# Performance work log

Hardware: AMD Instinct MI355X
Metric: run time of the kernel (lower is better)

## Reference

```python
import jax, jax.numpy as jnp
import numpy as np

N = 100000      # nodes
E_RAND = 1500000
IN_DIM = 128
OUT_DIM = 128
H = 8
D = OUT_DIM // H  # 16 per-head dim
EPS = 1e-5


def _bn(x, gamma, beta):
    # BatchNorm1d, training mode: biased batch statistics over the node dim
    mu = jnp.mean(x, axis=0)
    var = jnp.mean((x - mu) ** 2, axis=0)
    return (x - mu) * jax.lax.rsqrt(var + EPS) * gamma + beta


def setup_inputs() -> dict:
    key = jax.random.key(0)
    ks = jax.random.split(key, 12)
    h = jax.random.normal(ks[0], (N, IN_DIM), dtype=jnp.float32)
    # edge list: random edges + self-loops so every dst has in-degree >= 1
    src_r = jax.random.randint(ks[1], (E_RAND,), 0, N, dtype=jnp.int32)
    dst_r = jax.random.randint(ks[2], (E_RAND,), 0, N, dtype=jnp.int32)
    loops = jnp.arange(N, dtype=jnp.int32)
    src = jnp.concatenate([loops, src_r])
    dst = jnp.concatenate([loops, dst_r])
    s = 1.0 / np.sqrt(IN_DIM)
    Wq = jax.random.normal(ks[3], (IN_DIM, OUT_DIM), dtype=jnp.float32) * s
    Wk = jax.random.normal(ks[4], (IN_DIM, OUT_DIM), dtype=jnp.float32) * s
    Wv = jax.random.normal(ks[5], (IN_DIM, OUT_DIM), dtype=jnp.float32) * s
    Wo = jax.random.normal(ks[6], (OUT_DIM, OUT_DIM), dtype=jnp.float32) * s
    bo = jnp.zeros((OUT_DIM,), dtype=jnp.float32)
    gamma1 = jnp.ones((OUT_DIM,), dtype=jnp.float32)
    beta1 = jnp.zeros((OUT_DIM,), dtype=jnp.float32)
    Wf1 = jax.random.normal(ks[7], (OUT_DIM, 2 * OUT_DIM), dtype=jnp.float32) * s
    bf1 = jnp.zeros((2 * OUT_DIM,), dtype=jnp.float32)
    Wf2 = jax.random.normal(ks[8], (2 * OUT_DIM, OUT_DIM), dtype=jnp.float32) * (1.0 / np.sqrt(2 * OUT_DIM))
    bf2 = jnp.zeros((OUT_DIM,), dtype=jnp.float32)
    gamma2 = jnp.ones((OUT_DIM,), dtype=jnp.float32)
    beta2 = jnp.zeros((OUT_DIM,), dtype=jnp.float32)
    return {"h": h, "Wq": Wq, "Wk": Wk, "Wv": Wv, "Wo": Wo, "bo": bo,
            "gamma1": gamma1, "beta1": beta1, "Wf1": Wf1, "bf1": bf1,
            "Wf2": Wf2, "bf2": bf2, "gamma2": gamma2, "beta2": beta2,
            "src": src, "dst": dst}


def reference(h, Wq, Wk, Wv, Wo, bo, gamma1, beta1, Wf1, bf1, Wf2, bf2,
              gamma2, beta2, src, dst):
    n = h.shape[0]
    Q = (h @ Wq).reshape(n, H, D)
    K = (h @ Wk).reshape(n, H, D)
    V = (h @ Wv).reshape(n, H, D)
    # per-edge score: (K[src] * Q[dst]).sum(-1), scaled exp with clamp
    score = jnp.sum(K[src] * Q[dst], axis=-1) / np.sqrt(D)   # [E, H]
    score = jnp.exp(jnp.clip(score, -5.0, 5.0))
    # weighted aggregation to dst nodes
    wV = jax.ops.segment_sum(V[src] * score[:, :, None], dst, num_segments=n)  # [N,H,D]
    z = jax.ops.segment_sum(score, dst, num_segments=n)                         # [N,H]
    attn = (wV / z[:, :, None]).reshape(n, OUT_DIM)
    # output projection + residual + batchnorm
    x = h + (attn @ Wo + bo)
    x = _bn(x, gamma1, beta1)
    # FFN + residual + batchnorm
    y = jax.nn.relu(x @ Wf1 + bf1) @ Wf2 + bf2
    x = _bn(x + y, gamma2, beta2)
    return x
```

## Files before the change

### kernel.cpp

```cpp
#include <hip/hip_runtime.h>

#define EPS 1e-5f
#define VSCALE 20.0f

typedef __attribute__((ext_vector_type(8))) short sh8;
typedef __attribute__((ext_vector_type(4))) float f4;
typedef __attribute__((ext_vector_type(2))) _Float16 h2f;

static __device__ __forceinline__ unsigned short f2b(float f) {
    union { float f; unsigned u; } v; v.f = f;
    unsigned r = v.u + 0x7FFF + ((v.u >> 16) & 1);
    return (unsigned short)(r >> 16);
}
static __device__ __forceinline__ float b2f(unsigned short b) {
    union { unsigned u; float f; } v; v.u = ((unsigned)b) << 16; return v.f;
}
static __device__ __forceinline__ unsigned pk2(float a, float b) {
    return (unsigned)f2b(a) | ((unsigned)f2b(b) << 16);
}
static __device__ __forceinline__ h2f u2h(unsigned u) {
    union { unsigned u; h2f h; } c; c.u = u; return c.h;
}
static __device__ __forceinline__ float dot2h(h2f a, h2f b, float c) {
#if __has_builtin(__builtin_amdgcn_fdot2)
    return __builtin_amdgcn_fdot2(a, b, c, false);
#else
    return (float)a.x * (float)b.x + (float)a.y * (float)b.y + c;
#endif
}
#if __has_builtin(__builtin_amdgcn_cvt_f32_ubyte0)
#define UB0(x) __builtin_amdgcn_cvt_f32_ubyte0(x)
#define UB1(x) __builtin_amdgcn_cvt_f32_ubyte1(x)
#define UB2(x) __builtin_amdgcn_cvt_f32_ubyte2(x)
#define UB3(x) __builtin_amdgcn_cvt_f32_ubyte3(x)
#else
#define UB0(x) ((float)((x) & 0xffu))
#define UB1(x) ((float)(((x) >> 8) & 0xffu))
#define UB2(x) ((float)(((x) >> 16) & 0xffu))
#define UB3(x) ((float)((x) >> 24))
#endif

static __device__ __forceinline__ void barrier_raw() {
    __builtin_amdgcn_sched_barrier(0);
    asm volatile("s_waitcnt lgkmcnt(0)" ::: "memory");
    __builtin_amdgcn_s_barrier();
    __builtin_amdgcn_sched_barrier(0);
}

__global__ __launch_bounds__(256) void prep_all_k(
    const float* __restrict__ Wq, const float* __restrict__ Wk,
    const float* __restrict__ Wv, const float* __restrict__ Wo,
    const float* __restrict__ Wf1, const float* __restrict__ Wf2,
    unsigned short* __restrict__ Wt)
{
    int i = blockIdx.x * 256 + threadIdx.x;
    if (i < 65536) {
        int s = i >> 14;
        const float* W = (s == 0) ? Wq : (s == 1) ? Wk : (s == 2) ? Wv : Wo;
        int l = i & 16383, k = l >> 7, n = l & 127;
        Wt[(i & ~16383) + n * 128 + k] = f2b(W[l]);
    } else if (i < 98304) {
        int l = i - 65536, k = l >> 8, n = l & 255;
        Wt[65536 + n * 128 + k] = f2b(Wf1[l]);
    } else {
        int l = i - 98304, k = l >> 7, n = l & 127;
        Wt[98304 + n * 256 + k] = f2b(Wf2[l]);
    }
}

__global__ __launch_bounds__(256) void qkv_k(
    const float* __restrict__ h, const unsigned short* __restrict__ Wt,
    _Float16* __restrict__ Qh, unsigned char* __restrict__ KV, int M)
{
    __shared__ __align__(16) unsigned short As[128 * 136];
    __shared__ __align__(16) unsigned short Ws[128 * 72];
    const int tid = threadIdx.x;
    const int wave = tid >> 6, lane = tid & 63;
    const int q = lane >> 4, lm = lane & 15;
    const int rowBase = blockIdx.x * 128;
    const int r0 = (wave & 1) * 64, c0 = (wave >> 1) * 64;

#pragma unroll
    for (int j = 0; j < 16; ++j) {
        int idx = tid + j * 256;
        int row = idx >> 5, kk = (idx & 31) * 4;
        int grow = rowBase + row;
        float4 v = make_float4(0.f, 0.f, 0.f, 0.f);
        if (grow < M) v = *(const float4*)&h[(size_t)grow * 128 + kk];
        ushort4 b;
        b.x = f2b(v.x); b.y = f2b(v.y); b.z = f2b(v.z); b.w = f2b(v.w);
        *(ushort4*)&As[row * 136 + kk] = b;
    }

    for (int w = 0; w < 3; ++w) {
        f4 acc[4][4];
#pragma unroll
        for (int mi = 0; mi < 4; ++mi)
#pragma unroll
            for (int ni = 0; ni < 4; ++ni) {
                f4 z = {0.f, 0.f, 0.f, 0.f};
                acc[mi][ni] = z;
            }
        for (int kc = 0; kc < 2; ++kc) {
#pragma unroll
            for (int j = 0; j < 4; ++j) {
                int idx = tid + j * 256;
                int n = idx >> 3, kk = (idx & 7) * 8;
                uint4 v = *(const uint4*)&Wt[(size_t)w * 16384 + (size_t)n * 128 + kc * 64 + kk];
                *(uint4*)&Ws[n * 72 + kk] = v;
            }
            __syncthreads();
#pragma unroll
            for (int k2 = 0; k2 < 2; ++k2) {
                sh8 af[4], bfr[4];
#pragma unroll
                for (int t = 0; t < 4; ++t) {
                    af[t]  = *(const sh8*)&As[(r0 + t * 16 + lm) * 136 + kc * 64 + k2 * 32 + q * 8];
                    bfr[t] = *(const sh8*)&Ws[(c0 + t * 16 + lm) * 72 + k2 * 32 + q * 8];
                }
#pragma unroll
                for (int mi = 0; mi < 4; ++mi)
#pragma unroll
                    for (int ni = 0; ni < 4; ++ni)
                        acc[mi][ni] = __builtin_amdgcn_mfma_f32_16x16x32_bf16(
                            af[mi], bfr[ni], acc[mi][ni], 0, 0, 0);
            }
            __syncthreads();
        }
#pragma unroll
        for (int mi = 0; mi < 4; ++mi)
#pragma unroll
            for (int ni = 0; ni < 4; ++ni) {
                const int col = c0 + ni * 16 + lm;
#pragma unroll
                for (int r = 0; r < 4; ++r) {
                    int grow = rowBase + r0 + mi * 16 + q * 4 + r;
                    if (grow >= M) continue;
                    const float v = acc[mi][ni][r];
                    if (w == 0) Qh[(size_t)grow * 128 + col] = (_Float16)v;
                    else if (w == 1)
                        *(_Float16*)(KV + (size_t)grow * 384 + col * 2) = (_Float16)v;
                    else {
                        float t = rintf(v * VSCALE);
                        t = fminf(fmaxf(t, -127.f), 127.f);
                        KV[(size_t)grow * 384 + 256 + col] = (unsigned char)(int)(t + 128.f);
                    }
                }
            }
    }
}

template<int KD, int RES, int STATS, int RELU>
__global__ __launch_bounds__(512) void gemm2_k(
    const unsigned short* __restrict__ A, const unsigned short* __restrict__ Wt,
    const float* __restrict__ bias, const void* __restrict__ resid,
    unsigned short* __restrict__ C, int M, int ldc, int tiles,
    const float* __restrict__ aff1, float* __restrict__ ostats)
{
    constexpr int CPR = KD / 8;
    constexpr int PER = 64 * CPR / 512;
    __shared__ __align__(16) unsigned short Ws[128 * KD];
    __shared__ __align__(16) unsigned short As[2][64 * KD];
    __shared__ float sacc[256];
    const int tid = threadIdx.x;
    const int wave = tid >> 6, lane = tid & 63;
    const int q = lane >> 4, lm = lane & 15;
    const int wr = wave >> 2, wc = wave & 3;
    const int colBase = blockIdx.y * 128;
    const unsigned short* Wblk = Wt + (size_t)colBase * KD;

    uint4 rA[PER];
    {
        const int rowT = blockIdx.x * 64;
#pragma unroll
        for (int i = 0; i < PER; ++i) {
            int g = tid + i * 512;
            int row = g / CPR, ch = g % CPR;
            int grow = rowT + row; if (grow >= M) grow = M - 1;
            rA[i] = *(const uint4*)&A[(size_t)grow * KD + ch * 8];
        }
    }

#pragma unroll
    for (int i = 0; i < 128 * CPR / 512; ++i) {
        int g = tid + i * 512;
        int col = g / CPR, ch = g % CPR;
        uint4 v = *(const uint4*)&Wblk[(size_t)col * KD + ch * 8];
        *(uint4*)&Ws[col * KD + ((ch ^ (col & 7)) * 8)] = v;
    }
    if (STATS && tid < 256) sacc[tid] = 0.f;

    float bv[2], rsc[2], rsh[2];
#pragma unroll
    for (int ni = 0; ni < 2; ++ni) {
        const int col = colBase + wc * 32 + ni * 16 + lm;
        bv[ni] = bias[col];
        if (RES == 3) { rsc[ni] = aff1[col]; rsh[ni] = aff1[128 + col]; }
        else { rsc[ni] = 0.f; rsh[ni] = 0.f; }
    }
    float st_s[2] = {0.f, 0.f}, st_ss[2] = {0.f, 0.f};

    int cur = 0;
    for (int t = blockIdx.x; t < tiles; t += gridDim.x) {
        const int rowT = t * 64;
        barrier_raw();
        unsigned short* Asc = As[cur];
#pragma unroll
        for (int i = 0; i < PER; ++i) {
            int g = tid + i * 512;
            int row = g / CPR, ch = g % CPR;
            *(uint4*)&Asc[row * KD + ((ch ^ (row & 7)) * 8)] = rA[i];
        }
        const int tn = t + (int)gridDim.x;
        if (tn < tiles) {
            const int rowTn = tn * 64;
#pragma unroll
            for (int i = 0; i < PER; ++i) {
                int g = tid + i * 512;
                int row = g / CPR, ch = g % CPR;
                int grow = rowTn + row; if (grow >= M) grow = M - 1;
                rA[i] = *(const uint4*)&A[(size_t)grow * KD + ch * 8];
            }
        }
        barrier_raw();

        f4 acc[2][2];
#pragma unroll
        for (int mi = 0; mi < 2; ++mi)
#pragma unroll
            for (int ni = 0; ni < 2; ++ni) {
                f4 z = {0.f, 0.f, 0.f, 0.f};
                acc[mi][ni] = z;
            }
#pragma unroll
        for (int kc = 0; kc < KD / 32; ++kc) {
            sh8 af[2], bfr[2];
#pragma unroll
            for (int mi = 0; mi < 2; ++mi) {
                const int row = wr * 32 + mi * 16 + lm;
                af[mi] = *(const sh8*)&Asc[row * KD + (((kc * 4 + q) ^ (row & 7)) * 8)];
            }
#pragma unroll
            for (int ni = 0; ni < 2; ++ni) {
                const int col = wc * 32 + ni * 16 + lm;
                bfr[ni] = *(const sh8*)&Ws[col * KD + (((kc * 4 + q) ^ (col & 7)) * 8)];
            }
#pragma unroll
            for (int mi = 0; mi < 2; ++mi)
#pragma unroll
                for (int ni = 0; ni < 2; ++ni)
                    acc[mi][ni] = __builtin_amdgcn_mfma_f32_16x16x32_bf16(
                        af[mi], bfr[ni], acc[mi][ni], 0, 0, 0);
        }

#pragma unroll
        for (int ni = 0; ni < 2; ++ni) {
            const int col = colBase + wc * 32 + ni * 16 + lm;
#pragma unroll
            for (int mi = 0; mi < 2; ++mi) {
#pragma unroll
                for (int r = 0; r < 4; ++r) {
                    const int row = rowT + wr * 32 + mi * 16 + q * 4 + r;
                    if (row >= M) continue;
                    float val = acc[mi][ni][r] + bv[ni];
                    if (RES == 1)
                        val += ((const float*)resid)[(size_t)row * ldc + col];
                    if (RES == 3)
                        val += b2f(((const unsigned short*)resid)[(size_t)row * ldc + col])
                               * rsc[ni] + rsh[ni];
                    if (RELU) val = fmaxf(val, 0.f);
                    if (STATS) { st_s[ni] += val; st_ss[ni] += val * val; }
                    C[(size_t)row * ldc + col] = f2b(val);
                }
            }
        }
        cur ^= 1;
    }

    if (STATS) {
        barrier_raw();
#pragma unroll
        for (int ni = 0; ni < 2; ++ni) {
            st_s[ni]  += __shfl_xor(st_s[ni], 16);  st_s[ni]  += __shfl_xor(st_s[ni], 32);
            st_ss[ni] += __shfl_xor(st_ss[ni], 16); st_ss[ni] += __shfl_xor(st_ss[ni], 32);
            if (q == 0) {
                const int c = wc * 32 + ni * 16 + lm;
                atomicAdd(&sacc[c], st_s[ni]);
                atomicAdd(&sacc[128 + c], st_ss[ni]);
            }
        }
        barrier_raw();
        if (tid < 128) {
            atomicAdd(&ostats[tid], sacc[tid]);
            atomicAdd(&ostats[128 + tid], sacc[128 + tid]);
        }
    }
}

__global__ __launch_bounds__(256) void fold_bn1_k(
    const unsigned short* __restrict__ W1t, const float* __restrict__ rstats,
    const float* __restrict__ g1, const float* __restrict__ b1,
    const float* __restrict__ bf1, float invN,
    unsigned short* __restrict__ W1f, float* __restrict__ b1f,
    float* __restrict__ aff1)
{
    __shared__ float sc[128], sh[128];
    const int t = threadIdx.x;
    if (t < 128) {
        const float mu = rstats[t] * invN;
        const float var = rstats[128 + t] * invN - mu * mu;
        const float isg = rsqrtf(var + EPS) * g1[t];
        const float shf = b1[t] - mu * isg;
        sc[t] = isg; sh[t] = shf;
        aff1[t] = isg; aff1[128 + t] = shf;
    }
    __syncthreads();
    float acc = bf1[t];
#pragma unroll
    for (int c = 0; c < 128; c += 8) {
        const uint4 v = *(const uint4*)&W1t[t * 128 + c];
        const float w0 = b2f((unsigned short)(v.x & 0xffff));
        const float w1 = b2f((unsigned short)(v.x >> 16));
        const float w2 = b2f((unsigned short)(v.y & 0xffff));
        const float w3 = b2f((unsigned short)(v.y >> 16));
        const float w4 = b2f((unsigned short)(v.z & 0xffff));
        const float w5 = b2f((unsigned short)(v.z >> 16));
        const float w6 = b2f((unsigned short)(v.w & 0xffff));
        const float w7 = b2f((unsigned short)(v.w >> 16));
        acc += sh[c] * w0 + sh[c + 1] * w1 + sh[c + 2] * w2 + sh[c + 3] * w3
             + sh[c + 4] * w4 + sh[c + 5] * w5 + sh[c + 6] * w6 + sh[c + 7] * w7;
        uint4 o;
        o.x = pk2(w0 * sc[c],     w1 * sc[c + 1]);
        o.y = pk2(w2 * sc[c + 2], w3 * sc[c + 3]);
        o.z = pk2(w4 * sc[c + 4], w5 * sc[c + 5]);
        o.w = pk2(w6 * sc[c + 6], w7 * sc[c + 7]);
        *(uint4*)&W1f[t * 128 + c] = o;
    }
    b1f[t] = acc;
}

__global__ __launch_bounds__(256) void bucket_cnt_k(const int* __restrict__ dst,
                                                    int E, int* __restrict__ bCnt)
{
    __shared__ int c[512];
    const int t = threadIdx.x;
    c[t] = 0; c[t + 256] = 0;
    __syncthreads();
    for (int i = blockIdx.x * 256 + t; i < E; i += gridDim.x * 256)
        atomicAdd(&c[dst[i] >> 8], 1);
    __syncthreads();
    if (c[t]) atomicAdd(&bCnt[t], c[t]);
    if (c[t + 256]) atomicAdd(&bCnt[t + 256], c[t + 256]);
}

__global__ __launch_bounds__(512) void bucket_scan_k(const int* __restrict__ bCnt,
                                                     int B, int* __restrict__ bOff,
                                                     int* __restrict__ bCur)
{
    __shared__ int ts[512];
    const int t = threadIdx.x;
    const int v = (t < B) ? bCnt[t] : 0;
    ts[t] = v;
    __syncthreads();
    for (int o = 1; o < 512; o <<= 1) {
        int u = (t >= o) ? ts[t - o] : 0;
        __syncthreads();
        ts[t] += u;
        __syncthreads();
    }
    const int ex = ts[t] - v;
    if (t < B) { bOff[t] = ex; bCur[t] = ex; }
    if (t == B - 1) bOff[B] = ex + v;
}

#define CCH 8192
__global__ __launch_bounds__(512) void coarse_k(const int* __restrict__ src,
                                                const int* __restrict__ dst, int E,
                                                int* __restrict__ bCur,
                                                unsigned* __restrict__ coarse)
{
    __shared__ int cnt[512], off[512], gbase[512], rc[512];
    __shared__ unsigned pk[CCH];
    __shared__ int ga[CCH];
    const int t = threadIdx.x;
    const int e0 = blockIdx.x * CCH;
    const int n = min(CCH, E - e0);
    cnt[t] = 0;
    __syncthreads();
    for (int i = t; i < n; i += 512) atomicAdd(&cnt[dst[e0 + i] >> 8], 1);
    __syncthreads();
    const int v = cnt[t];
    off[t] = v;
    __syncthreads();
    for (int o = 1; o < 512; o <<= 1) {
        int u = (t >= o) ? off[t - o] : 0;
        __syncthreads();
        off[t] += u;
        __syncthreads();
    }
    const int ex = off[t] - v;
    off[t] = ex;
    if (v > 0) gbase[t] = atomicAdd(&bCur[t], v);
    rc[t] = 0;
    __syncthreads();
    for (int i = t; i < n; i += 512) {
        const int d = dst[e0 + i], s = src[e0 + i];
        const int b = d >> 8;
        const int j = atomicAdd(&rc[b], 1);
        const int slot = off[b] + j;
        pk[slot] = ((unsigned)(d & 255) << 17) | (unsigned)s;
        ga[slot] = gbase[b] + j;
    }
    __syncthreads();
    for (int i = t; i < n; i += 512) coarse[ga[i]] = pk[i];
}

__global__ __launch_bounds__(256) void fine_k(const unsigned* __restrict__ coarse,
                                              const int* __restrict__ bOff, int B,
                                              int Nn, int* __restrict__ row_ptr,
                                              int* __restrict__ esrc)
{
    __shared__ int cnt[256], off[256], rc[256];
    const int t = threadIdx.x;
    const int b = blockIdx.x;
    const int base = b << 8;
    const int e0 = bOff[b], e1 = bOff[b + 1];
    cnt[t] = 0;
    __syncthreads();
    for (int i = e0 + t; i < e1; i += 256)
        atomicAdd(&cnt[(coarse[i] >> 17) & 255], 1);
    __syncthreads();
    const int v = cnt[t];
    off[t] = v;
    __syncthreads();
    for (int o = 1; o < 256; o <<= 1) {
        int u = (t >= o) ? off[t - o] : 0;
        __syncthreads();
        off[t] += u;
        __syncthreads();
    }
    const int ex = off[t] - v;
    off[t] = ex;
    rc[t] = 0;
    if (base + t < Nn) row_ptr[base + t] = e0 + ex;
    if (b == B - 1 && t == 0) row_ptr[Nn] = e1;
    __syncthreads();
    for (int i = e0 + t; i < e1; i += 256) {
        const unsigned p = coarse[i];
        const int l = (p >> 17) & 255;
        const int j = atomicAdd(&rc[l], 1);
        esrc[e0 + off[l] + j] = (int)(p & 0x1FFFFu);
    }
}

#define EA_ACC(kc, vc, EI) do {                                              \
    float sp = dot2h(u2h((kc).w), q3, dot2h(u2h((kc).z), q2,                 \
               dot2h(u2h((kc).y), q1, dot2h(u2h((kc).x), q0, 0.f))));        \
    sp += __shfl_xor(sp, 1);                                                 \
    float sc = __expf(fminf(fmaxf(sp * 0.25f, -5.f), 5.f));                  \
    sc = ((EI) < nb) ? sc : 0.f;                                             \
    a0 += sc * UB0((vc).x);                                                  \
    a1 += sc * UB1((vc).x);                                                  \
    a2 += sc * UB2((vc).x);                                                  \
    a3 += sc * UB3((vc).x);                                                  \
    a4 += sc * UB0((vc).y);                                                  \
    a5 += sc * UB1((vc).y);                                                  \
    a6 += sc * UB2((vc).y);                                                  \
    a7 += sc * UB3((vc).y);                                                  \
    z += sc;                                                                 \
} while (0)

__global__ __launch_bounds__(256) void edge_attn_k(
    const _Float16* __restrict__ Qh, const unsigned char* __restrict__ KV,
    const int* __restrict__ row_ptr, const int* __restrict__ esrc,
    unsigned short* __restrict__ attnb, int Nn)
{
    const int wave = threadIdx.x >> 6, lane = threadIdx.x & 63;
    const int node = blockIdx.x * 4 + wave;
    if (node >= Nn) return;
    const int g = lane & 15, p = lane >> 4;
    const uint4 qv = *(const uint4*)&Qh[(size_t)node * 128 + g * 8];
    const h2f q0 = u2h(qv.x), q1 = u2h(qv.y), q2 = u2h(qv.z), q3 = u2h(qv.w);
    const int e0 = row_ptr[node], e1 = row_ptr[node + 1];
    const int cnt = e1 - e0;
    const int e1m1 = e1 - 1;
    float a0 = 0.f, a1 = 0.f, a2 = 0.f, a3 = 0.f;
    float a4 = 0.f, a5 = 0.f, a6 = 0.f, a7 = 0.f, z = 0.f;
    for (int base = 0; base < cnt; base += 64) {
        const int nb = min(cnt - base, 64);
        const int eb = e0 + base + p;
        {
            const int s0 = esrc[min(eb, e1m1)];
            const unsigned char* r = KV + (size_t)((unsigned)s0 * 384u);
            const int s1 = esrc[min(eb + 4, e1m1)];
            const unsigned char* rB = KV + (size_t)((unsigned)s1 * 384u);
            uint4 kvA = *(const uint4*)(r + g * 16);
            uint2 vvA = *(const uint2*)(r + 256 + g * 8);
            uint4 kvB = *(const uint4*)(rB + g * 16);
            uint2 vvB = *(const uint2*)(rB + 256 + g * 8);
            for (int j = 0; j < nb; j += 8) {
                {
                    const uint4 kc = kvA; const uint2 vc = vvA;
                    if (j + 8 < nb) {
                        const int sn = esrc[min(eb + j + 8, e1m1)];
                        const unsigned char* rn = KV + (size_t)((unsigned)sn * 384u);
                        kvA = *(const uint4*)(rn + g * 16);
                        vvA = *(const uint2*)(rn + 256 + g * 8);
                    }
                    EA_ACC(kc, vc, j + p);
                }
                {
                    const uint4 kc = kvB; const uint2 vc = vvB;
                    if (j + 12 < nb) {
                        const int sn = esrc[min(eb + j + 12, e1m1)];
                        const unsigned char* rn = KV + (size_t)((unsigned)sn * 384u);
                        kvB = *(const uint4*)(rn + g * 16);
                        vvB = *(const uint2*)(rn + 256 + g * 8);
                    }
                    EA_ACC(kc, vc, j + 4 + p);
                }
            }
        }
    }
    a0 += __shfl_xor(a0, 16); a0 += __shfl_xor(a0, 32);
    a1 += __shfl_xor(a1, 16); a1 += __shfl_xor(a1, 32);
    a2 += __shfl_xor(a2, 16); a2 += __shfl_xor(a2, 32);
    a3 += __shfl_xor(a3, 16); a3 += __shfl_xor(a3, 32);
    a4 += __shfl_xor(a4, 16); a4 += __shfl_xor(a4, 32);
    a5 += __shfl_xor(a5, 16); a5 += __shfl_xor(a5, 32);
    a6 += __shfl_xor(a6, 16); a6 += __shfl_xor(a6, 32);
    a7 += __shfl_xor(a7, 16); a7 += __shfl_xor(a7, 32);
    z  += __shfl_xor(z, 16);  z  += __shfl_xor(z, 32);
    const float inv = 1.f / (z * VSCALE);
    const float c = 128.f * z;
    if (p == 0) {
        uint4 o;
        o.x = pk2((a0 - c) * inv, (a1 - c) * inv);
        o.y = pk2((a2 - c) * inv, (a3 - c) * inv);
        o.z = pk2((a4 - c) * inv, (a5 - c) * inv);
        o.w = pk2((a6 - c) * inv, (a7 - c) * inv);
        *(uint4*)&attnb[(size_t)node * 128 + g * 8] = o;
    }
}

__global__ __launch_bounds__(256) void bn_apply_b_k(const unsigned short* __restrict__ X,
                                                    const float* __restrict__ rstats,
                                                    const float* __restrict__ gma,
                                                    const float* __restrict__ bta,
                                                    float invN, int total8,
                                                    float* __restrict__ out)
{
    __shared__ float aff[256];
    if (threadIdx.x < 128) {
        const int c = threadIdx.x;
        const float mu = rstats[c] * invN;
        const float var = rstats[128 + c] * invN - mu * mu;
        const float isg = rsqrtf(var + EPS) * gma[c];
        aff[c] = isg;
        aff[128 + c] = bta[c] - mu * isg;
    }
    __syncthreads();
    for (int i = blockIdx.x * blockDim.x + threadIdx.x; i < total8;
         i += gridDim.x * blockDim.x) {
        const int c8 = (i & 15) * 8;
        const float4 sc0 = *(const float4*)&aff[c8];
        const float4 sc1 = *(const float4*)&aff[c8 + 4];
        const float4 sh0 = *(const float4*)&aff[128 + c8];
        const float4 sh1 = *(const float4*)&aff[128 + c8 + 4];
        const uint4 v = ((const uint4*)X)[i];
        float4 o0, o1;
        o0.x = b2f((unsigned short)(v.x & 0xffff)) * sc0.x + sh0.x;
        o0.y = b2f((unsigned short)(v.x >> 16))    * sc0.y + sh0.y;
        o0.z = b2f((unsigned short)(v.y & 0xffff)) * sc0.z + sh0.z;
        o0.w = b2f((unsigned short)(v.y >> 16))    * sc0.w + sh0.w;
        o1.x = b2f((unsigned short)(v.z & 0xffff)) * sc1.x + sh1.x;
        o1.y = b2f((unsigned short)(v.z >> 16))    * sc1.y + sh1.y;
        o1.z = b2f((unsigned short)(v.w & 0xffff)) * sc1.z + sh1.z;
        o1.w = b2f((unsigned short)(v.w >> 16))    * sc1.w + sh1.w;
        ((float4*)out)[i * 2]     = o0;
        ((float4*)out)[i * 2 + 1] = o1;
    }
}

extern "C" void kernel_launch(void* const* d_in, const int* in_sizes, int n_in,
                              void* d_out, int out_size, void* d_ws, size_t ws_size,
                              hipStream_t stream)
{
    const float* h   = (const float*)d_in[0];
    const float* Wq  = (const float*)d_in[1];
    const float* Wk  = (const float*)d_in[2];
    const float* Wv  = (const float*)d_in[3];
    const float* Wo  = (const float*)d_in[4];
    const float* bo  = (const float*)d_in[5];
    const float* g1  = (const float*)d_in[6];
    const float* b1  = (const float*)d_in[7];
    const float* Wf1 = (const float*)d_in[8];
    const float* bf1 = (const float*)d_in[9];
    const float* Wf2 = (const float*)d_in[10];
    const float* bf2 = (const float*)d_in[11];
    const float* g2  = (const float*)d_in[12];
    const float* b2  = (const float*)d_in[13];
    const int*   src = (const int*)d_in[14];
    const int*   dstv= (const int*)d_in[15];
    const int N = in_sizes[0] / 128;
    const int E = in_sizes[14];
    const int B = (N + 255) >> 8;
    const float invN = 1.f / (float)N;

    unsigned short* Wt = (unsigned short*)d_ws;
    float* stats1 = (float*)((char*)d_ws + 262144);
    float* stats2 = stats1 + 256;
    int* bCnt = (int*)(stats2 + 256);
    int* bOff = bCnt + 512;
    int* bCur = bOff + 513;
    uintptr_t big = ((uintptr_t)(bCur + 512) + 255) & ~(uintptr_t)255;
    _Float16* Qh = (_Float16*)big;
    unsigned char* KV = (unsigned char*)(Qh + (size_t)N * 128);
    uintptr_t a2 = ((uintptr_t)(KV + (size_t)N * 384) + 255) & ~(uintptr_t)255;
    unsigned short* attnb = (unsigned short*)a2;
    unsigned short* xb = attnb + (size_t)N * 128;
    int* row_ptr = (int*)(xb + (size_t)N * 128);
    unsigned* coarse = (unsigned*)attnb;
    int* esrc = (int*)xb;
    unsigned short* hidden = (unsigned short*)Qh;
    unsigned short* yb = attnb;
    uintptr_t fb = (big + (size_t)N * 512 + 255) & ~(uintptr_t)255;
    float* aff1 = (float*)fb;
    float* b1f  = aff1 + 256;
    unsigned short* W1f = (unsigned short*)(b1f + 256);

    unsigned short* Wf1T = Wt + 65536;
    unsigned short* Wf2T = Wt + 98304;

    float* out = (float*)d_out;
    const dim3 b256(256);
    const dim3 b512(512);
    const int tiles128 = (N + 127) / 128;
    const int tiles64 = (N + 63) / 64;

    hipMemsetAsync(stats1, 0, 4096, stream);

    prep_all_k<<<dim3(512), b256, 0, stream>>>(Wq, Wk, Wv, Wo, Wf1, Wf2, Wt);

    bucket_cnt_k<<<dim3(256), b256, 0, stream>>>(dstv, E, bCnt);
    bucket_scan_k<<<dim3(1), dim3(512), 0, stream>>>(bCnt, B, bOff, bCur);
    coarse_k<<<dim3((E + CCH - 1) / CCH), dim3(512), 0, stream>>>(src, dstv, E, bCur, coarse);
    fine_k<<<dim3(B), b256, 0, stream>>>(coarse, bOff, B, N, row_ptr, esrc);

    qkv_k<<<dim3(tiles128), b256, 0, stream>>>(h, Wt, Qh, KV, N);

    edge_attn_k<<<dim3((N + 3) / 4), b256, 0, stream>>>(Qh, KV, row_ptr, esrc, attnb, N);

    gemm2_k<128, 1, 1, 0><<<dim3(512, 1), b512, 0, stream>>>(
        attnb, Wt + 49152, bo, h, xb, N, 128, tiles64, nullptr, stats1);

    fold_bn1_k<<<dim3(1), b256, 0, stream>>>(Wf1T, stats1, g1, b1, bf1, invN,
                                             W1f, b1f, aff1);

    gemm2_k<128, 0, 0, 1><<<dim3(512, 2), b512, 0, stream>>>(
        xb, W1f, b1f, nullptr, hidden, N, 256, tiles64, nullptr, nullptr);

    gemm2_k<256, 3, 1, 0><<<dim3(256, 1), b512, 0, stream>>>(
        hidden, Wf2T, bf2, xb, yb, N, 128, tiles64, aff1, stats2);

    bn_apply_b_k<<<dim3(1024), b256, 0, stream>>>(yb, stats2, g2, b2, invN, N * 16, out);
}
```

Measured before the change: 521.3 us.

## Rewrite QKV projection as persistent grid with resident weights and prefetched input

```diff
diff --git a/kernel.cpp b/kernel.cpp
--- a/kernel.cpp
+++ b/kernel.cpp
@@ -68,85 +68,125 @@
     }
 }
 
-__global__ __launch_bounds__(256) void qkv_k(
+__global__ __launch_bounds__(512, 4) void qkv3_k(
     const float* __restrict__ h, const unsigned short* __restrict__ Wt,
-    _Float16* __restrict__ Qh, unsigned char* __restrict__ KV, int M)
-{
-    __shared__ __align__(16) unsigned short As[128 * 136];
-    __shared__ __align__(16) unsigned short Ws[128 * 72];
+    _Float16* __restrict__ Qh, unsigned char* __restrict__ KV,
+    int M, int tiles)
+{
+    constexpr int KD = 128, CPR = 16, PER = 2;
+    __shared__ __align__(16) unsigned short Ws[128 * KD];
+    __shared__ __align__(16) unsigned short As[2][64 * KD];
     const int tid = threadIdx.x;
     const int wave = tid >> 6, lane = tid & 63;
     const int q = lane >> 4, lm = lane & 15;
-    const int rowBase = blockIdx.x * 128;
-    const int r0 = (wave & 1) * 64, c0 = (wave >> 1) * 64;
-
-#pragma unroll
-    for (int j = 0; j < 16; ++j) {
-        int idx = tid + j * 256;
-        int row = idx >> 5, kk = (idx & 31) * 4;
-        int grow = rowBase + row;
-        float4 v = make_float4(0.f, 0.f, 0.f, 0.f);
-        if (grow < M) v = *(const float4*)&h[(size_t)grow * 128 + kk];
-        ushort4 b;
-        b.x = f2b(v.x); b.y = f2b(v.y); b.z = f2b(v.z); b.w = f2b(v.w);
-        *(ushort4*)&As[row * 136 + kk] = b;
-    }
-
-    for (int w = 0; w < 3; ++w) {
-        f4 acc[4][4];
-#pragma unroll
-        for (int mi = 0; mi < 4; ++mi)
-#pragma unroll
-            for (int ni = 0; ni < 4; ++ni) {
+    const int wr = wave >> 2, wc = wave & 3;
+    const int wv = blockIdx.y;
+    const unsigned short* Wblk = Wt + (size_t)wv * 16384;
+
+    float4 rAf[PER][2];
+    {
+        const int rowT = blockIdx.x * 64;
+#pragma unroll
+        for (int i = 0; i < PER; ++i) {
+            int g = tid + i * 512;
+            int row = g >> 4, ch = g & 15;
+            int grow = rowT + row; if (grow >= M) grow = M - 1;
+            const float* p = &h[(size_t)grow * 128 + ch * 8];
+            rAf[i][0] = *(const float4*)p;
+            rAf[i][1] = *(const float4*)(p + 4);
+        }
+    }
+
+#pragma unroll
+    for (int i = 0; i < 4; ++i) {
+        int g = tid + i * 512;
+        int col = g >> 4, ch = g & 15;
+        uint4 v = *(const uint4*)&Wblk[(size_t)col * KD + ch * 8];
+        *(uint4*)&Ws[col * KD + ((ch ^ (col & 7)) * 8)] = v;
+    }
+
+    int cur = 0;
+    for (int t = blockIdx.x; t < tiles; t += gridDim.x) {
+        const int rowT = t * 64;
+        barrier_raw();
+        unsigned short* Asc = As[cur];
+#pragma unroll
+        for (int i = 0; i < PER; ++i) {
+            int g = tid + i * 512;
+            int row = g >> 4, ch = g & 15;
+            uint4 v;
+            v.x = pk2(rAf[i][0].x, rAf[i][0].y);
+            v.y = pk2(rAf[i][0].z, rAf[i][0].w);
+            v.z = pk2(rAf[i][1].x, rAf[i][1].y);
+            v.w = pk2(rAf[i][1].z, rAf[i][1].w);
+            *(uint4*)&Asc[row * KD + ((ch ^ (row & 7)) * 8)] = v;
+        }
+        const int tn = t + (int)gridDim.x;
+        if (tn < tiles) {
+            const int rowTn = tn * 64;
+#pragma unroll
+            for (int i = 0; i < PER; ++i) {
+                int g = tid + i * 512;
+                int row = g >> 4, ch = g & 15;
+                int grow = rowTn + row; if (grow >= M) grow = M - 1;
+                const float* p = &h[(size_t)grow * 128 + ch * 8];
+                rAf[i][0] = *(const float4*)p;
+                rAf[i][1] = *(const float4*)(p + 4);
+            }
+        }
+        barrier_raw();
+
+        f4 acc[2][2];
+#pragma unroll
+        for (int mi = 0; mi < 2; ++mi)
+#pragma unroll
+            for (int ni = 0; ni < 2; ++ni) {
                 f4 z = {0.f, 0.f, 0.f, 0.f};
                 acc[mi][ni] = z;
             }
-        for (int kc = 0; kc < 2; ++kc) {
-#pragma unroll
-            for (int j = 0; j < 4; ++j) {
-                int idx = tid + j * 256;
-                int n = idx >> 3, kk = (idx & 7) * 8;
-                uint4 v = *(const uint4*)&Wt[(size_t)w * 16384 + (size_t)n * 128 + kc * 64 + kk];
-                *(uint4*)&Ws[n * 72 + kk] = v;
-            }
-            __syncthreads();
-#pragma unroll
-            for (int k2 = 0; k2 < 2; ++k2) {
-                sh8 af[4], bfr[4];
-#pragma unroll
-                for (int t = 0; t < 4; ++t) {
-                    af[t]  = *(const sh8*)&As[(r0 + t * 16 + lm) * 136 + kc * 64 + k2 * 32 + q * 8];
-                    bfr[t] = *(const sh8*)&Ws[(c0 + t * 16 + lm) * 72 + k2 * 32 + q * 8];
-                }
-#pragma unroll
-                for (int mi = 0; mi < 4; ++mi)
-#pragma unroll
-                    for (int ni = 0; ni < 4; ++ni)
-                        acc[mi][ni] = __builtin_amdgcn_mfma_f32_16x16x32_bf16(
-                            af[mi], bfr[ni], acc[mi][ni], 0, 0, 0);
-            }
-            __syncthreads();
-        }
-#pragma unroll
-        for (int mi = 0; mi < 4; ++mi)
-#pragma unroll
-            for (int ni = 0; ni < 4; ++ni) {
-                const int col = c0 + ni * 16 + lm;
+#pragma unroll
+        for (int kc = 0; kc < 4; ++kc) {
+            sh8 af[2], bfr[2];
+#pragma unroll
+            for (int mi = 0; mi < 2; ++mi) {
+                const int row = wr * 32 + mi * 16 + lm;
+                af[mi] = *(const sh8*)&Asc[row * KD + (((kc * 4 + q) ^ (row & 7)) * 8)];
+            }
+#pragma unroll
+            for (int ni = 0; ni < 2; ++ni) {
+                const int col = wc * 32 + ni * 16 + lm;
+                bfr[ni] = *(const sh8*)&Ws[col * KD + (((kc * 4 + q) ^ (col & 7)) * 8)];
+            }
+#pragma unroll
+            for (int mi = 0; mi < 2; ++mi)
+#pragma unroll
+                for (int ni = 0; ni < 2; ++ni)
+                    acc[mi][ni] = __builtin_amdgcn_mfma_f32_16x16x32_bf16(
+                        af[mi], bfr[ni], acc[mi][ni], 0, 0, 0);
+        }
+
+#pragma unroll
+        for (int ni = 0; ni < 2; ++ni) {
+            const int col = wc * 32 + ni * 16 + lm;
+#pragma unroll
+            for (int mi = 0; mi < 2; ++mi) {
 #pragma unroll
                 for (int r = 0; r < 4; ++r) {
-                    int grow = rowBase + r0 + mi * 16 + q * 4 + r;
-                    if (grow >= M) continue;
+                    const int row = rowT + wr * 32 + mi * 16 + q * 4 + r;
+                    if (row >= M) continue;
                     const float v = acc[mi][ni][r];
-                    if (w == 0) Qh[(size_t)grow * 128 + col] = (_Float16)v;
-                    else if (w == 1)
-                        *(_Float16*)(KV + (size_t)grow * 384 + col * 2) = (_Float16)v;
+                    if (wv == 0) Qh[(size_t)row * 128 + col] = (_Float16)v;
+                    else if (wv == 1)
+                        *(_Float16*)(KV + (size_t)row * 384 + col * 2) = (_Float16)v;
                     else {
-                        float t = rintf(v * VSCALE);
-                        t = fminf(fmaxf(t, -127.f), 127.f);
-                        KV[(size_t)grow * 384 + 256 + col] = (unsigned char)(int)(t + 128.f);
+                        float tt = rintf(v * VSCALE);
+                        tt = fminf(fmaxf(tt, -127.f), 127.f);
+                        KV[(size_t)row * 384 + 256 + col] = (unsigned char)(int)(tt + 128.f);
                     }
                 }
             }
+        }
+        cur ^= 1;
     }
 }
 
@@ -635,7 +675,6 @@
     float* out = (float*)d_out;
     const dim3 b256(256);
     const dim3 b512(512);
-    const int tiles128 = (N + 127) / 128;
     const int tiles64 = (N + 63) / 64;
 
     hipMemsetAsync(stats1, 0, 4096, stream);
@@ -647,7 +686,7 @@
     coarse_k<<<dim3((E + CCH - 1) / CCH), dim3(512), 0, stream>>>(src, dstv, E, bCur, coarse);
     fine_k<<<dim3(B), b256, 0, stream>>>(coarse, bOff, B, N, row_ptr, esrc);
 
-    qkv_k<<<dim3(tiles128), b256, 0, stream>>>(h, Wt, Qh, KV, N);
+    qkv3_k<<<dim3(171, 3), b512, 0, stream>>>(h, Wt, Qh, KV, N, tiles64);
 
     edge_attn_k<<<dim3((N + 3) / 4), b256, 0, stream>>>(Qh, KV, row_ptr, esrc, attnb, N);
 
```

Result: faster. 475.2 us (-8.9%).
